# Kernel tuning notes

Measured on AMD Instinct MI355X. Metric: run time of the kernel, lower is better.

## Reference

```python
import jax, jax.numpy as jnp
import numpy as np

B, T, I, H = 32, 512, 1024, 1024


def setup_inputs() -> dict:
    key = jax.random.key(0)
    k1, k2, k3 = jax.random.split(key, 3)
    s_w = 1.0 / np.sqrt(I)
    s_u = 1.0 / np.sqrt(H)
    return {
        "x": jax.random.normal(k1, (B, T, I), dtype=jnp.float32),
        "W": jax.random.normal(k2, (4 * H, I), dtype=jnp.float32) * s_w,
        "b_w": jnp.zeros((4 * H,), dtype=jnp.float32),
        "U": jax.random.normal(k3, (4 * H, H), dtype=jnp.float32) * s_u,
        "b_u": jnp.zeros((4 * H,), dtype=jnp.float32),
    }


def reference(x, W, b_w, U, b_u):
    # x: [B, T, I]; W: [4H, I]; U: [4H, H]
    Bn, Tn, _ = x.shape
    Hn = U.shape[1]
    # Precompute input projection for all timesteps (as in the torch module)
    wx = jnp.einsum("bti,gi->btg", x, W) + b_w  # [B, T, 4H]
    Ut = U.T  # [H, 4H]

    def step(carry, wx_t):
        h, c = carry
        gates = wx_t + h @ Ut + b_u          # [B, 4H]
        i, f, g, o = jnp.split(gates, 4, axis=-1)
        c = jax.nn.sigmoid(f) * c + jax.nn.sigmoid(i) * jnp.tanh(g)
        # eval-mode drop mask is 1.0; nonlinearity='relu' on cell state
        h = jax.nn.sigmoid(o) * jax.nn.relu(c)
        return (h, c), (h, c)

    h0 = jnp.zeros((Bn, Hn), dtype=x.dtype)
    c0 = jnp.zeros((Bn, Hn), dtype=x.dtype)
    (_, _), (hs, cs) = jax.lax.scan(step, (h0, c0), jnp.swapaxes(wx, 0, 1))
    # [T, B, H] -> [B, T, H]
    return jnp.swapaxes(hs, 0, 1), jnp.swapaxes(cs, 0, 1)
```

## Files before the change

kernel.cpp:

```cpp
#include <hip/hip_runtime.h>
#include <hip/hip_bf16.h>

#define B_  32
#define T_  512
#define I_  1024
#define H_  1024
#define G4_ 4096
#define NWG 32

typedef short short8 __attribute__((ext_vector_type(8)));
typedef float f32x4  __attribute__((ext_vector_type(4)));

__device__ __forceinline__ ushort f2bf(float f) {
    unsigned u = __builtin_bit_cast(unsigned, f);
    u += 0x7fffu + ((u >> 16) & 1u);
    return (ushort)(u >> 16);
}
__device__ __forceinline__ float bf2f(ushort u) {
    unsigned x = ((unsigned)u) << 16;
    return __builtin_bit_cast(float, x);
}

__device__ __forceinline__ void async16(const void* g, void* l) {
    __builtin_amdgcn_global_load_lds((const __attribute__((address_space(1))) void*)g,
                                     (__attribute__((address_space(3))) void*)l,
                                     16, 0, 0);
}

__global__ void cvt_bf16(const float* __restrict__ in, ushort* __restrict__ out, int n) {
    int stride = gridDim.x * blockDim.x;
    for (int i = blockIdx.x * blockDim.x + threadIdx.x; i * 4 < n; i += stride) {
        float4 v = reinterpret_cast<const float4*>(in)[i];
        ushort4 o;
        o.x = f2bf(v.x); o.y = f2bf(v.y); o.z = f2bf(v.z); o.w = f2bf(v.w);
        reinterpret_cast<ushort4*>(out)[i] = o;
    }
}

#define BM 128
#define BN 128
#define BK 32

__global__ __launch_bounds__(256) void gemm_bt(
    const ushort* __restrict__ A, const ushort* __restrict__ Bm,
    const float* __restrict__ bias, ushort* __restrict__ C,
    int M, int N, int K)
{
    __shared__ ushort sA[2][BM * BK];
    __shared__ ushort sB[2][BN * BK];

    const int tid  = threadIdx.x;
    const int m0   = blockIdx.y * BM;
    const int n0   = blockIdx.x * BN;
    const int lane = tid & 63, wid = tid >> 6;
    const int wm   = (wid >> 1) * 64, wn = (wid & 1) * 64;
    const int lr   = lane & 15, lg = lane >> 4;

    f32x4 acc[4][4] = {};

    auto stage = [&](int buf, int kt) {
        const int k0 = kt * BK;
#pragma unroll
        for (int i = 0; i < 2; ++i) {
            int c = tid + i * 256;
            const ushort* ga = A  + (size_t)(m0 + (c >> 2)) * K + k0 + (c & 3) * 8;
            async16(ga, &sA[buf][c * 8]);
            const ushort* gb = Bm + (size_t)(n0 + (c >> 2)) * K + k0 + (c & 3) * 8;
            async16(gb, &sB[buf][c * 8]);
        }
    };

    stage(0, 0);
    __syncthreads();

    const int nk = K / BK;
    int buf = 0;
    for (int kt = 0; kt < nk; ++kt) {
        if (kt + 1 < nk) stage(buf ^ 1, kt + 1);
        short8 af[4], bfr[4];
#pragma unroll
        for (int i = 0; i < 4; ++i)
            af[i]  = *reinterpret_cast<const short8*>(&sA[buf][(wm + i * 16 + lr) * BK + lg * 8]);
#pragma unroll
        for (int i = 0; i < 4; ++i)
            bfr[i] = *reinterpret_cast<const short8*>(&sB[buf][(wn + i * 16 + lr) * BK + lg * 8]);
#pragma unroll
        for (int mi = 0; mi < 4; ++mi)
#pragma unroll
            for (int ni = 0; ni < 4; ++ni)
                acc[mi][ni] = __builtin_amdgcn_mfma_f32_16x16x32_bf16(af[mi], bfr[ni], acc[mi][ni], 0, 0, 0);
        __syncthreads();
        buf ^= 1;
    }

#pragma unroll
    for (int mi = 0; mi < 4; ++mi) {
#pragma unroll
        for (int ni = 0; ni < 4; ++ni) {
            int col = n0 + wn + ni * 16 + lr;
            float bv = bias[col];
#pragma unroll
            for (int r = 0; r < 4; ++r) {
                int row = m0 + wm + mi * 16 + lg * 4 + r;
                int b = row >> 9, t = row & (T_ - 1);
                C[((size_t)t * B_ + b) * G4_ + col] = f2bf(acc[mi][ni][r] + bv);
            }
        }
    }
}

__global__ __launch_bounds__(512, 2) void lstm_persist(
    const ushort* __restrict__ wx,
    const ushort* __restrict__ U_bf,
    const float*  __restrict__ b_u,
    ushort* __restrict__ hb0,
    ushort* __restrict__ hb1,
    float*  __restrict__ hs,
    float*  __restrict__ cs,
    unsigned* __restrict__ cnt)
{
    const int tid = threadIdx.x;
    const int lane = tid & 63, wid = tid >> 6;
    const int lr = lane & 15, lg = lane >> 4;
    const int g = wid & 3, hh = wid >> 2;
    const int j = blockIdx.x;
    const int colh = j * 32 + hh * 16 + lr;
    const int colg = g * H_ + colh;

    short8 ureg[32];
    {
        const ushort* up = U_bf + (size_t)colg * H_ + lg * 8;
#pragma unroll
        for (int k = 0; k < 32; ++k)
            ureg[k] = *reinterpret_cast<const short8*>(up + k * 32);
    }
    const float bu = b_u[colg];

    __shared__ ushort sh[32 * 1024];
    __shared__ float  gates[4][32][32];

    const int b0p = tid >> 5, ci0 = tid & 31;
    float creg0 = 0.f, creg1 = 0.f;

    for (int t = 0; t < T_; ++t) {
        if (t > 0) {
            if (tid == 0) {
                while (atomicAdd(cnt, 0u) < (unsigned)(NWG * t)) {
                    __builtin_amdgcn_s_sleep(2);
                }
                __threadfence();
            }
            __syncthreads();

            const char* hpc = (const char*)((t & 1) ? hb0 : hb1);
#pragma unroll
            for (int i = 0; i < 8; ++i) {
                int o = (i * 512 + tid) * 16;
                int row = o >> 11, inner = o & 2047;
                int si = inner ^ ((row & 7) << 4);
                async16(hpc + row * 2048 + si, ((char*)sh) + o);
            }
            __syncthreads();

            f32x4 acc0 = {}, acc1 = {};
            const char* shc = (const char*)sh;
            const int sw = (lr & 7) << 4;
            const int base0 = lr * 2048, base1 = (16 + lr) * 2048;
#pragma unroll
            for (int k = 0; k < 32; ++k) {
                int cb = (k * 32 + lg * 8) * 2;
                short8 a0 = *reinterpret_cast<const short8*>(shc + base0 + (cb ^ sw));
                short8 a1 = *reinterpret_cast<const short8*>(shc + base1 + (cb ^ sw));
                acc0 = __builtin_amdgcn_mfma_f32_16x16x32_bf16(a0, ureg[k], acc0, 0, 0, 0);
                acc1 = __builtin_amdgcn_mfma_f32_16x16x32_bf16(a1, ureg[k], acc1, 0, 0, 0);
            }
            const ushort* wxt = wx + (size_t)t * B_ * G4_;
#pragma unroll
            for (int r = 0; r < 4; ++r) {
                gates[g][lg * 4 + r][hh * 16 + lr] =
                    acc0[r] + bf2f(wxt[(lg * 4 + r) * G4_ + colg]) + bu;
                gates[g][16 + lg * 4 + r][hh * 16 + lr] =
                    acc1[r] + bf2f(wxt[(16 + lg * 4 + r) * G4_ + colg]) + bu;
            }
        } else {
            const ushort* wxt = wx;
#pragma unroll
            for (int r = 0; r < 4; ++r) {
                gates[g][lg * 4 + r][hh * 16 + lr] =
                    bf2f(wxt[(lg * 4 + r) * G4_ + colg]) + bu;
                gates[g][16 + lg * 4 + r][hh * 16 + lr] =
                    bf2f(wxt[(16 + lg * 4 + r) * G4_ + colg]) + bu;
            }
        }
        __syncthreads();

        ushort* hn = (t & 1) ? hb1 : hb0;
        {
            int col = j * 32 + ci0;
            float gi = gates[0][b0p][ci0], gf = gates[1][b0p][ci0];
            float gg = gates[2][b0p][ci0], go = gates[3][b0p][ci0];
            float si = 1.f / (1.f + __expf(-gi));
            float sf = 1.f / (1.f + __expf(-gf));
            float so = 1.f / (1.f + __expf(-go));
            float tg = 2.f / (1.f + __expf(-2.f * gg)) - 1.f;
            float c  = sf * creg0 + si * tg;  creg0 = c;
            float h  = so * fmaxf(c, 0.f);
            hn[b0p * H_ + col] = f2bf(h);
            hs[((size_t)b0p * T_ + t) * H_ + col] = h;
            cs[((size_t)b0p * T_ + t) * H_ + col] = c;

            int b1 = 16 + b0p;
            gi = gates[0][b1][ci0]; gf = gates[1][b1][ci0];
            gg = gates[2][b1][ci0]; go = gates[3][b1][ci0];
            si = 1.f / (1.f + __expf(-gi));
            sf = 1.f / (1.f + __expf(-gf));
            so = 1.f / (1.f + __expf(-go));
            tg = 2.f / (1.f + __expf(-2.f * gg)) - 1.f;
            c  = sf * creg1 + si * tg;  creg1 = c;
            h  = so * fmaxf(c, 0.f);
            hn[b1 * H_ + col] = f2bf(h);
            hs[((size_t)b1 * T_ + t) * H_ + col] = h;
            cs[((size_t)b1 * T_ + t) * H_ + col] = c;
        }

        __syncthreads();
        if (tid == 0) {
            __threadfence();
            atomicAdd(cnt, 1u);
        }
    }
}

extern "C" void kernel_launch(void* const* d_in, const int* in_sizes, int n_in,
                              void* d_out, int out_size, void* d_ws, size_t ws_size,
                              hipStream_t stream)
{
    const float* x  = (const float*)d_in[0];
    const float* W  = (const float*)d_in[1];
    const float* bw = (const float*)d_in[2];
    const float* Uf = (const float*)d_in[3];
    const float* bu = (const float*)d_in[4];

    float* out = (float*)d_out;
    float* hs  = out;
    float* cs  = out + (size_t)B_ * T_ * H_;

    char* ws = (char*)d_ws;
    ushort*  x_bf  = (ushort*)ws;
    ushort*  W_bf  = (ushort*)(ws + 33554432);
    ushort*  U_bf  = (ushort*)(ws + 41943040);
    ushort*  wx_bf = (ushort*)(ws + 50331648);
    ushort*  hb0   = (ushort*)(ws + 184549376);
    ushort*  hb1   = (ushort*)(ws + 184614912);
    unsigned* cnt  = (unsigned*)(ws + 184680448);

    hipMemsetAsync(cnt, 0, 256, stream);

    cvt_bf16<<<2048, 256, 0, stream>>>(x,  x_bf, B_ * T_ * I_);
    cvt_bf16<<<1024, 256, 0, stream>>>(W,  W_bf, G4_ * I_);
    cvt_bf16<<<1024, 256, 0, stream>>>(Uf, U_bf, G4_ * H_);

    dim3 grid(G4_ / BN, (B_ * T_) / BM);
    gemm_bt<<<grid, 256, 0, stream>>>(x_bf, W_bf, bw, wx_bf, B_ * T_, G4_, I_);

    lstm_persist<<<NWG, 512, 0, stream>>>(wx_bf, U_bf, bu, hb0, hb1, hs, cs, cnt);
}
```

Baseline: 4.662 ms.

## Split K across waves, prefetch wx asynchronously, use relaxed atomics for h exchange

Restructures the persistent LSTM step so each wave computes two 16-column tiles over half of K, with the partial sums reduced through swizzled shared memory. The wx slice for the next step is prefetched into LDS asynchronously, replacing per-step strided global loads. The h exchange now uses relaxed agent-scope atomic loads and stores instead of async LDS loads, threadfences and atomicAdd polling. Elementwise work now handles two packed columns per thread, with non-temporal 64-bit stores for hs/cs issued after the barrier signal. The aim is to shorten the serial per-step critical path. Dropping the fences relies on the relaxed atomics and the barrier being enough to order the h writes before the counter update.

```diff
diff --git a/kernel.cpp b/kernel.cpp
--- a/kernel.cpp
+++ b/kernel.cpp
@@ -111,123 +111,144 @@
 
 __global__ __launch_bounds__(512, 2) void lstm_persist(
     const ushort* __restrict__ wx,
-    const ushort* __restrict__ U_bf,
+    const ushort* U_bf,
     const float*  __restrict__ b_u,
-    ushort* __restrict__ hb0,
-    ushort* __restrict__ hb1,
+    uint*   __restrict__ hbuf,
     float*  __restrict__ hs,
     float*  __restrict__ cs,
-    unsigned* __restrict__ cnt)
+    unsigned* cnt)
 {
-    const int tid = threadIdx.x;
+    const int tid  = threadIdx.x;
     const int lane = tid & 63, wid = tid >> 6;
-    const int lr = lane & 15, lg = lane >> 4;
-    const int g = wid & 3, hh = wid >> 2;
-    const int j = blockIdx.x;
-    const int colh = j * 32 + hh * 16 + lr;
-    const int colg = g * H_ + colh;
-
-    short8 ureg[32];
-    {
-        const ushort* up = U_bf + (size_t)colg * H_ + lg * 8;
-#pragma unroll
-        for (int k = 0; k < 32; ++k)
-            ureg[k] = *reinterpret_cast<const short8*>(up + k * 32);
-    }
-    const float bu = b_u[colg];
+    const int lr   = lane & 15, lg = lane >> 4;
+    const int g    = wid & 3, kh = wid >> 2;
+    const int j    = blockIdx.x;
+
+    short8 ureg[2][16];
+#pragma unroll
+    for (int n = 0; n < 2; ++n)
+#pragma unroll
+        for (int s = 0; s < 16; ++s) {
+            const volatile uint* p =
+                (const volatile uint*)(U_bf + (size_t)(g * 1024 + j * 32 + n * 16 + lr) * 1024
+                                       + kh * 512 + s * 32 + lg * 8);
+            uint4 w; w.x = p[0]; w.y = p[1]; w.z = p[2]; w.w = p[3];
+            ureg[n][s] = __builtin_bit_cast(short8, w);
+        }
 
     __shared__ ushort sh[32 * 1024];
-    __shared__ float  gates[4][32][32];
-
-    const int b0p = tid >> 5, ci0 = tid & 31;
-    float creg0 = 0.f, creg1 = 0.f;
+    __shared__ float  gpart[2][4][32][32];
+    __shared__ ushort swx[2][4096];
+    char* shc = (char*)sh;
+
+    const int bp = tid >> 4, cp = (tid & 15) * 2;
+    float creg[2] = {0.f, 0.f};
+    float bu2[4][2];
+#pragma unroll
+    for (int g2 = 0; g2 < 4; ++g2) {
+        bu2[g2][0] = b_u[g2 * 1024 + j * 32 + cp];
+        bu2[g2][1] = b_u[g2 * 1024 + j * 32 + cp + 1];
+    }
+
+    auto prefetch_wx = [&](int tt, int buf) {
+        int b = tid >> 4, g2 = (tid >> 2) & 3, q = tid & 3;
+        const ushort* src = wx + ((size_t)tt * 32 + b) * 4096 + g2 * 1024 + j * 32 + q * 8;
+        async16(src, (char*)swx + buf * 8192 + tid * 16);
+    };
+
+    prefetch_wx(0, 0);
 
     for (int t = 0; t < T_; ++t) {
         if (t > 0) {
             if (tid == 0) {
-                while (atomicAdd(cnt, 0u) < (unsigned)(NWG * t)) {
-                    __builtin_amdgcn_s_sleep(2);
+                while (__hip_atomic_load(cnt, __ATOMIC_RELAXED, __HIP_MEMORY_SCOPE_AGENT)
+                       < (unsigned)(NWG * t))
+                    __builtin_amdgcn_s_sleep(1);
+            }
+            __syncthreads();
+
+            const unsigned long long* hsrc =
+                (const unsigned long long*)(hbuf + ((t + 1) & 1) * 16384);
+#pragma unroll
+            for (int i = 0; i < 16; ++i) {
+                int idx = i * 512 + tid;
+                unsigned long long v = __hip_atomic_load(&hsrc[idx],
+                    __ATOMIC_RELAXED, __HIP_MEMORY_SCOPE_AGENT);
+                int o = idx * 8, row = o >> 11, inner = o & 2047;
+                *(unsigned long long*)(shc + row * 2048 + (inner ^ ((row & 7) << 4))) = v;
+            }
+            __syncthreads();
+
+            prefetch_wx(t + 1 < T_ ? t + 1 : t, (t + 1) & 1);
+
+            f32x4 acc[2][2] = {};
+            const int swz = (lr & 7) << 4;
+#pragma unroll
+            for (int s = 0; s < 16; ++s) {
+                int kb = (kh * 512 + s * 32 + lg * 8) * 2;
+                short8 a0 = *(const short8*)(shc + lr * 2048 + (kb ^ swz));
+                short8 a1 = *(const short8*)(shc + (16 + lr) * 2048 + (kb ^ swz));
+#pragma unroll
+                for (int n = 0; n < 2; ++n) {
+                    acc[0][n] = __builtin_amdgcn_mfma_f32_16x16x32_bf16(a0, ureg[n][s], acc[0][n], 0, 0, 0);
+                    acc[1][n] = __builtin_amdgcn_mfma_f32_16x16x32_bf16(a1, ureg[n][s], acc[1][n], 0, 0, 0);
                 }
-                __threadfence();
-            }
-            __syncthreads();
-
-            const char* hpc = (const char*)((t & 1) ? hb0 : hb1);
-#pragma unroll
-            for (int i = 0; i < 8; ++i) {
-                int o = (i * 512 + tid) * 16;
-                int row = o >> 11, inner = o & 2047;
-                int si = inner ^ ((row & 7) << 4);
-                async16(hpc + row * 2048 + si, ((char*)sh) + o);
-            }
-            __syncthreads();
-
-            f32x4 acc0 = {}, acc1 = {};
-            const char* shc = (const char*)sh;
-            const int sw = (lr & 7) << 4;
-            const int base0 = lr * 2048, base1 = (16 + lr) * 2048;
-#pragma unroll
-            for (int k = 0; k < 32; ++k) {
-                int cb = (k * 32 + lg * 8) * 2;
-                short8 a0 = *reinterpret_cast<const short8*>(shc + base0 + (cb ^ sw));
-                short8 a1 = *reinterpret_cast<const short8*>(shc + base1 + (cb ^ sw));
-                acc0 = __builtin_amdgcn_mfma_f32_16x16x32_bf16(a0, ureg[k], acc0, 0, 0, 0);
-                acc1 = __builtin_amdgcn_mfma_f32_16x16x32_bf16(a1, ureg[k], acc1, 0, 0, 0);
-            }
-            const ushort* wxt = wx + (size_t)t * B_ * G4_;
-#pragma unroll
-            for (int r = 0; r < 4; ++r) {
-                gates[g][lg * 4 + r][hh * 16 + lr] =
-                    acc0[r] + bf2f(wxt[(lg * 4 + r) * G4_ + colg]) + bu;
-                gates[g][16 + lg * 4 + r][hh * 16 + lr] =
-                    acc1[r] + bf2f(wxt[(16 + lg * 4 + r) * G4_ + colg]) + bu;
-            }
+            }
+#pragma unroll
+            for (int m = 0; m < 2; ++m)
+#pragma unroll
+                for (int n = 0; n < 2; ++n) {
+                    int col = n * 16 + lr;
+                    int bb  = (m * 16 + lg * 4) ^ ((col & 7) << 2);
+                    *(f32x4*)&gpart[kh][g][col][bb] = acc[m][n];
+                }
         } else {
-            const ushort* wxt = wx;
-#pragma unroll
-            for (int r = 0; r < 4; ++r) {
-                gates[g][lg * 4 + r][hh * 16 + lr] =
-                    bf2f(wxt[(lg * 4 + r) * G4_ + colg]) + bu;
-                gates[g][16 + lg * 4 + r][hh * 16 + lr] =
-                    bf2f(wxt[(16 + lg * 4 + r) * G4_ + colg]) + bu;
-            }
+            prefetch_wx(1, 1);
         }
         __syncthreads();
 
-        ushort* hn = (t & 1) ? hb1 : hb0;
-        {
-            int col = j * 32 + ci0;
-            float gi = gates[0][b0p][ci0], gf = gates[1][b0p][ci0];
-            float gg = gates[2][b0p][ci0], go = gates[3][b0p][ci0];
-            float si = 1.f / (1.f + __expf(-gi));
-            float sf = 1.f / (1.f + __expf(-gf));
-            float so = 1.f / (1.f + __expf(-go));
-            float tg = 2.f / (1.f + __expf(-2.f * gg)) - 1.f;
-            float c  = sf * creg0 + si * tg;  creg0 = c;
-            float h  = so * fmaxf(c, 0.f);
-            hn[b0p * H_ + col] = f2bf(h);
-            hs[((size_t)b0p * T_ + t) * H_ + col] = h;
-            cs[((size_t)b0p * T_ + t) * H_ + col] = c;
-
-            int b1 = 16 + b0p;
-            gi = gates[0][b1][ci0]; gf = gates[1][b1][ci0];
-            gg = gates[2][b1][ci0]; go = gates[3][b1][ci0];
-            si = 1.f / (1.f + __expf(-gi));
-            sf = 1.f / (1.f + __expf(-gf));
-            so = 1.f / (1.f + __expf(-go));
-            tg = 2.f / (1.f + __expf(-2.f * gg)) - 1.f;
-            c  = sf * creg1 + si * tg;  creg1 = c;
-            h  = so * fmaxf(c, 0.f);
-            hn[b1 * H_ + col] = f2bf(h);
-            hs[((size_t)b1 * T_ + t) * H_ + col] = h;
-            cs[((size_t)b1 * T_ + t) * H_ + col] = c;
-        }
+        float hv[2], cv[2];
+        uint wxu[4];
+#pragma unroll
+        for (int g2 = 0; g2 < 4; ++g2)
+            wxu[g2] = *(const uint*)((const ushort*)swx + (t & 1) * 4096 + bp * 128 + g2 * 32 + cp);
+#pragma unroll
+        for (int cc = 0; cc < 2; ++cc) {
+            int col = cp + cc;
+            float gv[4];
+#pragma unroll
+            for (int g2 = 0; g2 < 4; ++g2) {
+                float s = bf2f((ushort)(cc ? (wxu[g2] >> 16) : (wxu[g2] & 0xffffu))) + bu2[g2][cc];
+                if (t > 0) {
+                    int bb = bp ^ ((col & 7) << 2);
+                    s += gpart[0][g2][col][bb] + gpart[1][g2][col][bb];
+                }
+                gv[g2] = s;
+            }
+            float si = 1.f / (1.f + __expf(-gv[0]));
+            float sf = 1.f / (1.f + __expf(-gv[1]));
+            float tg = 2.f / (1.f + __expf(-2.f * gv[2])) - 1.f;
+            float so = 1.f / (1.f + __expf(-gv[3]));
+            float c  = sf * creg[cc] + si * tg;
+            creg[cc] = c;
+            cv[cc]   = c;
+            hv[cc]   = so * fmaxf(c, 0.f);
+        }
+        uint hp = (uint)f2bf(hv[0]) | ((uint)f2bf(hv[1]) << 16);
+        __hip_atomic_store(&hbuf[(t & 1) * 16384 + bp * 512 + (j * 32 + cp) / 2], hp,
+                           __ATOMIC_RELAXED, __HIP_MEMORY_SCOPE_AGENT);
 
         __syncthreads();
-        if (tid == 0) {
-            __threadfence();
-            atomicAdd(cnt, 1u);
-        }
+        if (tid == 0)
+            __hip_atomic_fetch_add(cnt, 1u, __ATOMIC_RELAXED, __HIP_MEMORY_SCOPE_AGENT);
+
+        size_t ob = ((size_t)bp * T_ + t) * H_ + j * 32 + cp;
+        unsigned long long hq = (unsigned long long)__builtin_bit_cast(unsigned, hv[0])
+                              | ((unsigned long long)__builtin_bit_cast(unsigned, hv[1]) << 32);
+        unsigned long long cq = (unsigned long long)__builtin_bit_cast(unsigned, cv[0])
+                              | ((unsigned long long)__builtin_bit_cast(unsigned, cv[1]) << 32);
+        __builtin_nontemporal_store(hq, (unsigned long long*)(hs + ob));
+        __builtin_nontemporal_store(cq, (unsigned long long*)(cs + ob));
     }
 }
 
@@ -246,13 +267,12 @@
     float* cs  = out + (size_t)B_ * T_ * H_;
 
     char* ws = (char*)d_ws;
-    ushort*  x_bf  = (ushort*)ws;
-    ushort*  W_bf  = (ushort*)(ws + 33554432);
-    ushort*  U_bf  = (ushort*)(ws + 41943040);
-    ushort*  wx_bf = (ushort*)(ws + 50331648);
-    ushort*  hb0   = (ushort*)(ws + 184549376);
-    ushort*  hb1   = (ushort*)(ws + 184614912);
-    unsigned* cnt  = (unsigned*)(ws + 184680448);
+    ushort*   x_bf  = (ushort*)ws;
+    ushort*   W_bf  = (ushort*)(ws + 33554432);
+    ushort*   U_bf  = (ushort*)(ws + 41943040);
+    ushort*   wx_bf = (ushort*)(ws + 50331648);
+    uint*     hbuf  = (uint*)(ws + 184549376);
+    unsigned* cnt   = (unsigned*)(ws + 184680448);
 
     hipMemsetAsync(cnt, 0, 256, stream);
 
@@ -263,5 +283,5 @@
     dim3 grid(G4_ / BN, (B_ * T_) / BM);
     gemm_bt<<<grid, 256, 0, stream>>>(x_bf, W_bf, bw, wx_bf, B_ * T_, G4_, I_);
 
-    lstm_persist<<<NWG, 512, 0, stream>>>(wx_bf, U_bf, bu, hb0, hb1, hs, cs, cnt);
-}
+    lstm_persist<<<NWG, 512, 0, stream>>>(wx_bf, U_bf, bu, hbuf, hs, cs, cnt);
+}
```

Result: faster. 4.018 ms (-13.8%).
